# Kernel tuning notes

Measured on AMD Instinct MI355X. Metric: run time of the kernel, lower is better.

Reference implementation:

```python
import jax, jax.numpy as jnp
import numpy as np

N_P, E_P = 50000, 400000
N_L, E_L = 50000, 400000
B = 256  # number of graphs per side
NEG_GAT = 0.2   # GATv2 leaky-relu slope
NEG_FC = 0.01   # nn.LeakyReLU default slope


def _gatv2(x, ei, Wl, Wr, att, b, H, C):
    """GATv2Conv (concat heads, add_self_loops=True). Wl/Wr: [in, H*C], att: [H, C], b: [H*C]."""
    N = x.shape[0]
    sl = jnp.arange(N)
    src = jnp.concatenate([ei[0], sl])
    dst = jnp.concatenate([ei[1], sl])
    xl = (x @ Wl).reshape(N, H, C)   # source transform (messages)
    xr = (x @ Wr).reshape(N, H, C)   # target transform
    e = jax.nn.leaky_relu(xl[src] + xr[dst], NEG_GAT)          # [E+N, H, C]
    logits = jnp.einsum('ehc,hc->eh', e, att)                   # [E+N, H]
    m = jax.ops.segment_max(logits, dst, num_segments=N)        # segment softmax
    a = jnp.exp(logits - m[dst])
    alpha = a / jax.ops.segment_sum(a, dst, num_segments=N)[dst]
    out = jax.ops.segment_sum(xl[src] * alpha[..., None], dst, num_segments=N)
    return out.reshape(N, H * C) + b


def _mean_pool(x, batch, nb):
    s = jax.ops.segment_sum(x, batch, num_segments=nb)
    c = jax.ops.segment_sum(jnp.ones((x.shape[0],), x.dtype), batch, num_segments=nb)
    return s / jnp.maximum(c, 1.0)[:, None]


def setup_inputs() -> dict:
    key = jax.random.key(0)
    ks = jax.random.split(key, 48)
    i = [0]
    def nrm(shape, fan_in):
        k = ks[i[0]]; i[0] += 1
        return jax.random.normal(k, shape, jnp.float32) / np.sqrt(fan_in)
    inp = {}
    inp['protein_x'] = jax.random.normal(ks[40], (N_P, 10), jnp.float32)
    inp['ligand_x'] = jax.random.normal(ks[41], (N_L, 5), jnp.float32)
    inp['protein_edge_index'] = jax.random.randint(ks[42], (2, E_P), 0, N_P)
    inp['ligand_edge_index'] = jax.random.randint(ks[43], (2, E_L), 0, N_L)
    inp['protein_batch'] = (jnp.arange(N_P) * B) // N_P  # sorted graph ids, all segments nonempty
    inp['ligand_batch'] = (jnp.arange(N_L) * B) // N_L
    # GATv2 params: layer1 heads=2 out=128, layer2 heads=1 out=256
    inp['p1_Wl'] = nrm((10, 256), 10); inp['p1_Wr'] = nrm((10, 256), 10)
    inp['p1_att'] = nrm((2, 128), 128); inp['p1_b'] = jnp.zeros((256,), jnp.float32)
    inp['p2_Wl'] = nrm((256, 256), 256); inp['p2_Wr'] = nrm((256, 256), 256)
    inp['p2_att'] = nrm((1, 256), 256); inp['p2_b'] = jnp.zeros((256,), jnp.float32)
    inp['l1_Wl'] = nrm((5, 256), 5); inp['l1_Wr'] = nrm((5, 256), 5)
    inp['l1_att'] = nrm((2, 128), 128); inp['l1_b'] = jnp.zeros((256,), jnp.float32)
    inp['l2_Wl'] = nrm((256, 256), 256); inp['l2_Wr'] = nrm((256, 256), 256)
    inp['l2_att'] = nrm((1, 256), 256); inp['l2_b'] = jnp.zeros((256,), jnp.float32)
    # MultiheadAttention(256, 4) params ([in, out] convention)
    inp['Wq'] = nrm((256, 256), 256); inp['bq'] = jnp.zeros((256,), jnp.float32)
    inp['Wk'] = nrm((256, 256), 256); inp['bk'] = jnp.zeros((256,), jnp.float32)
    inp['Wv'] = nrm((256, 256), 256); inp['bv'] = jnp.zeros((256,), jnp.float32)
    inp['Wo'] = nrm((256, 256), 256); inp['bo'] = jnp.zeros((256,), jnp.float32)
    # fc head
    inp['fc1_w'] = nrm((512, 256), 512); inp['fc1_b'] = jnp.zeros((256,), jnp.float32)
    inp['ln_g'] = jnp.ones((256,), jnp.float32); inp['ln_b'] = jnp.zeros((256,), jnp.float32)
    inp['fc2_w'] = nrm((256, 1), 256); inp['fc2_b'] = jnp.zeros((1,), jnp.float32)
    return inp


def reference(protein_x, protein_edge_index, protein_batch,
              ligand_x, ligand_edge_index, ligand_batch,
              p1_Wl, p1_Wr, p1_att, p1_b, p2_Wl, p2_Wr, p2_att, p2_b,
              l1_Wl, l1_Wr, l1_att, l1_b, l2_Wl, l2_Wr, l2_att, l2_b,
              Wq, bq, Wk, bk, Wv, bv, Wo, bo,
              fc1_w, fc1_b, ln_g, ln_b, fc2_w, fc2_b):
    px = _gatv2(protein_x, protein_edge_index, p1_Wl, p1_Wr, p1_att, p1_b, 2, 128)
    px = _gatv2(px, protein_edge_index, p2_Wl, p2_Wr, p2_att, p2_b, 1, 256)
    px = _mean_pool(px, protein_batch, B)                        # [B, 256]
    lx = _gatv2(ligand_x, ligand_edge_index, l1_Wl, l1_Wr, l1_att, l1_b, 2, 128)
    lx = _gatv2(lx, ligand_edge_index, l2_Wl, l2_Wr, l2_att, l2_b, 1, 256)
    lx = _mean_pool(lx, ligand_batch, B)                         # [B, 256]
    # cross attention with q/k/v seq length 1
    D, H = 256, 4
    d = D // H
    qh = (px @ Wq + bq).reshape(B, H, d)
    kh = (lx @ Wk + bk).reshape(B, H, d)
    vh = (lx @ Wv + bv).reshape(B, H, d)
    scores = (qh * kh).sum(-1) / jnp.sqrt(jnp.float32(d))        # [B, H], 1 key
    w = jax.nn.softmax(scores[..., None], axis=-1)               # all ones (single key)
    attn = (w * vh).reshape(B, D) @ Wo + bo                      # [B, 256]
    comb = jnp.concatenate([px, attn], axis=1)                   # [B, 512]
    h = comb @ fc1_w + fc1_b
    mu = h.mean(-1, keepdims=True)
    var = h.var(-1, keepdims=True)
    h = (h - mu) / jnp.sqrt(var + 1e-5) * ln_g + ln_b
    h = jax.nn.leaky_relu(h, NEG_FC)
    return h @ fc2_w + fc2_b                                     # [B, 1]
```

## Files before the change

### kernel.cpp

```cpp
#include <hip/hip_runtime.h>
#include <math.h>

typedef unsigned short u16;
typedef __attribute__((ext_vector_type(8))) short bf16x8;
typedef __attribute__((ext_vector_type(4))) float f32x4;

__device__ inline u16 f2bf(float x) {
  unsigned int u = __float_as_uint(x);
  u += 0x7fffu + ((u >> 16) & 1u);
  return (u16)(u >> 16);
}
__device__ inline float bf2f(u16 h) {
  return __uint_as_float(((unsigned int)h) << 16);
}
__device__ inline float4 ld_bf4(const u16* p) {
  ushort4 v = *(const ushort4*)p;
  return make_float4(bf2f(v.x), bf2f(v.y), bf2f(v.z), bf2f(v.w));
}

__global__ void k_setup(int* __restrict__ cnt, int nz,
                        const float* __restrict__ Wpl, const float* __restrict__ Wpr,
                        const float* __restrict__ Wll, const float* __restrict__ Wlr,
                        u16* __restrict__ Whp, u16* __restrict__ Wlp,
                        u16* __restrict__ Whl, u16* __restrict__ Wll_o) {
  const int zb = (nz + 255) / 256;
  if ((int)blockIdx.x < zb) {
    int i = blockIdx.x * 256 + threadIdx.x;
    if (i < nz) cnt[i] = 0;
    return;
  }
  int wb = blockIdx.x - zb;
  int n = wb & 511;
  int side = wb >> 9;
  int col = n & 255;
  int k = threadIdx.x;
  const float* W = side == 0 ? (n < 256 ? Wpl : Wpr) : (n < 256 ? Wll : Wlr);
  float w = W[k * 256 + col];
  u16* Wh = side ? Whl : Whp;
  u16* Wlo = side ? Wll_o : Wlp;
  u16 hb = f2bf(w);
  Wh[n * 256 + k] = hb;
  Wlo[n * 256 + k] = f2bf(w - bf2f(hb));
}

__global__ void k_histb(const int* __restrict__ eip, int Ep, const int* __restrict__ eil,
                        int El, int* __restrict__ cntp, int* __restrict__ cntl) {
  int e = blockIdx.x * blockDim.x + threadIdx.x;
  if (e < Ep) atomicAdd(&cntp[eip[Ep + e]], 1);
  else if (e < Ep + El) { int e2 = e - Ep; atomicAdd(&cntl[eil[El + e2]], 1); }
}

__global__ void k_scan1b(const int* __restrict__ cntp, int Np, const int* __restrict__ cntl,
                         int Nl, int nbp, int* __restrict__ offsp, int* __restrict__ offsl,
                         int* __restrict__ curp, int* __restrict__ curl,
                         int* __restrict__ bsum) {
  __shared__ int s[256];
  int tid = threadIdx.x;
  int side = ((int)blockIdx.x >= nbp) ? 1 : 0;
  int blk = side ? (blockIdx.x - nbp) : blockIdx.x;
  const int* cnt = side ? cntl : cntp;
  int* offs = side ? offsl : offsp;
  int* cur = side ? curl : curp;
  int N = side ? Nl : Np;
  int i = blk * 256 + tid;
  int v = (i < N) ? cnt[i] : 0;
  if (i < N) cur[i] = 0;
  s[tid] = v;
  __syncthreads();
  for (int off = 1; off < 256; off <<= 1) {
    int t = 0;
    if (tid >= off) t = s[tid - off];
    __syncthreads();
    if (tid >= off) s[tid] += t;
    __syncthreads();
  }
  if (i < N) offs[i] = s[tid] - v;
  if (tid == 255) bsum[side * 256 + blk] = s[255];
}

__global__ void k_scan2b(int* __restrict__ bsum, int nbp, int nbl) {
  __shared__ int s[256];
  int side = blockIdx.x;
  int nb = side ? nbl : nbp;
  int* bs = bsum + side * 256;
  int tid = threadIdx.x;
  int v = (tid < nb) ? bs[tid] : 0;
  s[tid] = v;
  __syncthreads();
  for (int off = 1; off < 256; off <<= 1) {
    int t = 0;
    if (tid >= off) t = s[tid - off];
    __syncthreads();
    if (tid >= off) s[tid] += t;
    __syncthreads();
  }
  if (tid < nb) bs[tid] = s[tid] - v;
}

__global__ void k_fillb(const int* __restrict__ eip, int Ep, const int* __restrict__ eil,
                        int El, const int* __restrict__ offsp, const int* __restrict__ offsl,
                        const int* __restrict__ bsum,
                        int* __restrict__ curp, int* __restrict__ curl,
                        int* __restrict__ csrp, int* __restrict__ csrl) {
  int e = blockIdx.x * blockDim.x + threadIdx.x;
  if (e < Ep) {
    int d = eip[Ep + e];
    int pos = offsp[d] + bsum[d >> 8] + atomicAdd(&curp[d], 1);
    csrp[pos] = eip[e];
  } else if (e < Ep + El) {
    int e2 = e - Ep;
    int d = eil[El + e2];
    int pos = offsl[d] + bsum[256 + (d >> 8)] + atomicAdd(&curl[d], 1);
    csrl[pos] = eil[e2];
  }
}

__global__ void k_lin_small_b(const float* __restrict__ xp, int Kp, int Np,
                              const float* __restrict__ xl_, int Kl, int Nl,
                              const float* __restrict__ Wpl, const float* __restrict__ Wpr,
                              const float* __restrict__ Wll, const float* __restrict__ Wlr,
                              u16* __restrict__ xlh_p, u16* __restrict__ xrh_p,
                              u16* __restrict__ xlh_l, u16* __restrict__ xrh_l) {
  const int side = blockIdx.y;
  const float* x = side ? xl_ : xp;
  const int K = side ? Kl : Kp;
  const int N = side ? Nl : Np;
  const float* Wl = side ? Wll : Wpl;
  const float* Wr = side ? Wlr : Wpr;
  u16* xlh = side ? xlh_l : xlh_p;
  u16* xrh = side ? xrh_l : xrh_p;
  int base = blockIdx.x * 8;
  if (base >= N) return;
  int j = threadIdx.x;
  __shared__ float xs[8][16];
  int tot = 8 * K;
  for (int i = j; i < tot; i += 256) {
    int r = i / K, k = i - r * K;
    if (base + r < N) xs[r][k] = x[(size_t)(base + r) * K + k];
  }
  __syncthreads();
#pragma unroll
  for (int r = 0; r < 8; ++r) {
    int n = base + r;
    if (n >= N) break;
    float al = 0.f, ar = 0.f;
    for (int k = 0; k < K; ++k) {
      float xv = xs[r][k];
      al = fmaf(xv, Wl[k * 256 + j], al);
      ar = fmaf(xv, Wr[k * 256 + j], ar);
    }
    xlh[(size_t)n * 256 + j] = f2bf(al);
    xrh[(size_t)n * 256 + j] = f2bf(ar);
  }
}

__global__ void __launch_bounds__(256, 2) k_mm_dual_b(
    const u16* __restrict__ A_p, const u16* __restrict__ A_l,
    const u16* __restrict__ Bh_p, const u16* __restrict__ Bl_p,
    const u16* __restrict__ Bh_l, const u16* __restrict__ Bl_l,
    u16* __restrict__ XLh_p, u16* __restrict__ XRh_p,
    u16* __restrict__ XLh_l, u16* __restrict__ XRh_l, int Np, int Nl) {
  __shared__ __align__(16) char smem[32768];
  char* sA = smem;
  char* sBh = smem + 8192;
  char* sBl = smem + 16384;
  const int side = blockIdx.z;
  const u16* A = side ? A_l : A_p;
  const u16* Bhi = side ? Bh_l : Bh_p;
  const u16* Blo = side ? Bl_l : Bl_p;
  u16* XLh = side ? XLh_l : XLh_p;
  u16* XRh = side ? XRh_l : XRh_p;
  const int M = side ? Nl : Np;
  const int t = threadIdx.x;
  const int rowBase = blockIdx.x * 128;
  if (rowBase >= M) return;
  const int j0 = blockIdx.y * 128;
  const int srow = t >> 1;
  const int h = t & 1;
  int gr = rowBase + srow;
  if (gr >= M) gr = M - 1;
  const size_t gaBase = (size_t)gr * 256 + h * 16;
  const size_t gbBase = (size_t)(j0 + srow) * 256 + h * 16;
  const int rb = srow * 64;
  const int sw0 = (((h * 2) + (srow >> 1)) & 3) * 16;
  const int sw1 = (((h * 2 + 1) + (srow >> 1)) & 3) * 16;
  const int lane = t & 63;
  const int wid = t >> 6;
  const int wm = (wid & 1) * 64;
  const int wn = (wid >> 1) * 64;
  const int kq = lane >> 4;
  const int mr = lane & 15;
  int offA[4], offB[4];
#pragma unroll
  for (int i = 0; i < 4; ++i) {
    int m = wm + i * 16 + mr;
    offA[i] = m * 64 + ((kq + (m >> 1)) & 3) * 16;
    int n = wn + i * 16 + mr;
    offB[i] = n * 64 + ((kq + (n >> 1)) & 3) * 16;
  }
  f32x4 acc[4][4] = {};
  for (int kt = 0; kt < 8; ++kt) {
    const int k0 = kt * 32;
    uint4 va0 = *(const uint4*)(A + gaBase + k0);
    uint4 va1 = *(const uint4*)(A + gaBase + k0 + 8);
    uint4 vbh0 = *(const uint4*)(Bhi + gbBase + k0);
    uint4 vbh1 = *(const uint4*)(Bhi + gbBase + k0 + 8);
    uint4 vbl0 = *(const uint4*)(Blo + gbBase + k0);
    uint4 vbl1 = *(const uint4*)(Blo + gbBase + k0 + 8);
    __syncthreads();
    *(uint4*)(sA + rb + sw0) = va0;
    *(uint4*)(sA + rb + sw1) = va1;
    *(uint4*)(sBh + rb + sw0) = vbh0;
    *(uint4*)(sBh + rb + sw1) = vbh1;
    *(uint4*)(sBl + rb + sw0) = vbl0;
    *(uint4*)(sBl + rb + sw1) = vbl1;
    __syncthreads();
    bf16x8 a[4], bh[4], bl[4];
#pragma unroll
    for (int i = 0; i < 4; ++i) {
      a[i] = *(const bf16x8*)(sA + offA[i]);
      bh[i] = *(const bf16x8*)(sBh + offB[i]);
      bl[i] = *(const bf16x8*)(sBl + offB[i]);
    }
#pragma unroll
    for (int i = 0; i < 4; ++i)
#pragma unroll
      for (int j = 0; j < 4; ++j) {
        acc[i][j] = __builtin_amdgcn_mfma_f32_16x16x32_bf16(a[i], bh[j], acc[i][j], 0, 0, 0);
        acc[i][j] = __builtin_amdgcn_mfma_f32_16x16x32_bf16(a[i], bl[j], acc[i][j], 0, 0, 0);
      }
  }
  __syncthreads();
  u16* wtile = (u16*)(smem + wid * 8192);
#pragma unroll
  for (int i = 0; i < 4; ++i)
#pragma unroll
    for (int j = 0; j < 4; ++j)
#pragma unroll
      for (int r = 0; r < 4; ++r)
        wtile[(i * 16 + kq * 4 + r) * 64 + j * 16 + mr] = f2bf(acc[i][j][r]);
  u16* cbase = (blockIdx.y < 2) ? XLh : XRh;
  const int cb = (blockIdx.y < 2) ? j0 : j0 - 256;
  const int r8 = lane >> 3;
  const int c8 = lane & 7;
#pragma unroll
  for (int rr = 0; rr < 8; ++rr) {
    int lr = rr * 8 + r8;
    uint4 v = *(const uint4*)&wtile[lr * 64 + c8 * 8];
    int row = rowBase + wm + lr;
    if (row < M) *(uint4*)&cbase[(size_t)row * 256 + cb + wn + c8 * 8] = v;
  }
}

#define GAT_DOT(a, q)                                                        \
  {                                                                          \
    float t0 = a.x + rd.x, t1 = a.y + rd.y, t2 = a.z + rd.z, t3 = a.w + rd.w; \
    q = fmaf(fmaxf(t0, 0.2f * t0), wa.x,                                     \
        fmaf(fmaxf(t1, 0.2f * t1), wa.y,                                     \
        fmaf(fmaxf(t2, 0.2f * t2), wa.z, fmaxf(t3, 0.2f * t3) * wa.w)));     \
  }

template <int H>
__global__ void k_gat_gather_b(
    const u16* __restrict__ xlh_p, const u16* __restrict__ xrh_p, u16* __restrict__ out_p,
    const u16* __restrict__ xlh_l, const u16* __restrict__ xrh_l, u16* __restrict__ out_l,
    const int* __restrict__ csr_p, const int* __restrict__ offs_p,
    const int* __restrict__ cnt_p,
    const int* __restrict__ csr_l, const int* __restrict__ offs_l,
    const int* __restrict__ cnt_l, const int* __restrict__ bsum,
    const float* __restrict__ att_p, const float* __restrict__ bias_p,
    const float* __restrict__ att_l, const float* __restrict__ bias_l,
    int Np, int Nl) {
  const int side = blockIdx.y;
  const u16* xlh = side ? xlh_l : xlh_p;
  const u16* xrh = side ? xrh_l : xrh_p;
  u16* out = side ? out_l : out_p;
  const int* csr = side ? csr_l : csr_p;
  const int* offs = side ? offs_l : offs_p;
  const int* cnt = side ? cnt_l : cnt_p;
  const float* att = side ? att_l : att_p;
  const float* bias = side ? bias_l : bias_p;
  const int N = side ? Nl : Np;
  int d = blockIdx.x * 4 + (threadIdx.x >> 6);
  if (d >= N) return;
  const int lo4 = (threadIdx.x & 63) * 4;
  const float4 rd = ld_bf4(&xrh[(size_t)d * 256 + lo4]);
  const float4 wa = *(const float4*)&att[lo4];
  const float4 xd = ld_bf4(&xlh[(size_t)d * 256 + lo4]);
  float base;
  GAT_DOT(xd, base)
#pragma unroll
  for (int off = 1; off <= (H == 2 ? 16 : 32); off <<= 1) base += __shfl_xor(base, off, 64);
  float l0 = 1.f, l1 = 0.f, l2 = 0.f, l3 = 0.f;
  float4 acc0 = xd;
  float4 acc1 = make_float4(0.f, 0.f, 0.f, 0.f);
  float4 acc2 = make_float4(0.f, 0.f, 0.f, 0.f);
  float4 acc3 = make_float4(0.f, 0.f, 0.f, 0.f);
  const int o0 = offs[d] + bsum[side * 256 + (d >> 8)];
  const int c = cnt[d];
  int j = 0;
  for (; j + 3 < c; j += 4) {
    int s0 = csr[o0 + j], s1 = csr[o0 + j + 1], s2 = csr[o0 + j + 2], s3 = csr[o0 + j + 3];
    float4 a0 = ld_bf4(&xlh[(size_t)s0 * 256 + lo4]);
    float4 a1 = ld_bf4(&xlh[(size_t)s1 * 256 + lo4]);
    float4 a2 = ld_bf4(&xlh[(size_t)s2 * 256 + lo4]);
    float4 a3 = ld_bf4(&xlh[(size_t)s3 * 256 + lo4]);
    float q0, q1, q2, q3;
    GAT_DOT(a0, q0)
    GAT_DOT(a1, q1)
    GAT_DOT(a2, q2)
    GAT_DOT(a3, q3)
#pragma unroll
    for (int off = 1; off <= (H == 2 ? 16 : 32); off <<= 1) {
      q0 += __shfl_xor(q0, off, 64);
      q1 += __shfl_xor(q1, off, 64);
      q2 += __shfl_xor(q2, off, 64);
      q3 += __shfl_xor(q3, off, 64);
    }
    float w0 = __expf(q0 - base), w1 = __expf(q1 - base);
    float w2 = __expf(q2 - base), w3 = __expf(q3 - base);
    l0 += w0; l1 += w1; l2 += w2; l3 += w3;
    acc0.x = fmaf(w0, a0.x, acc0.x); acc0.y = fmaf(w0, a0.y, acc0.y);
    acc0.z = fmaf(w0, a0.z, acc0.z); acc0.w = fmaf(w0, a0.w, acc0.w);
    acc1.x = fmaf(w1, a1.x, acc1.x); acc1.y = fmaf(w1, a1.y, acc1.y);
    acc1.z = fmaf(w1, a1.z, acc1.z); acc1.w = fmaf(w1, a1.w, acc1.w);
    acc2.x = fmaf(w2, a2.x, acc2.x); acc2.y = fmaf(w2, a2.y, acc2.y);
    acc2.z = fmaf(w2, a2.z, acc2.z); acc2.w = fmaf(w2, a2.w, acc2.w);
    acc3.x = fmaf(w3, a3.x, acc3.x); acc3.y = fmaf(w3, a3.y, acc3.y);
    acc3.z = fmaf(w3, a3.z, acc3.z); acc3.w = fmaf(w3, a3.w, acc3.w);
  }
  for (; j < c; ++j) {
    int s0 = csr[o0 + j];
    float4 a0 = ld_bf4(&xlh[(size_t)s0 * 256 + lo4]);
    float q0;
    GAT_DOT(a0, q0)
#pragma unroll
    for (int off = 1; off <= (H == 2 ? 16 : 32); off <<= 1) q0 += __shfl_xor(q0, off, 64);
    float w0 = __expf(q0 - base);
    l0 += w0;
    acc0.x = fmaf(w0, a0.x, acc0.x); acc0.y = fmaf(w0, a0.y, acc0.y);
    acc0.z = fmaf(w0, a0.z, acc0.z); acc0.w = fmaf(w0, a0.w, acc0.w);
  }
  float inv = 1.f / (l0 + l1 + l2 + l3);
  float ax = acc0.x + acc1.x + acc2.x + acc3.x;
  float ay = acc0.y + acc1.y + acc2.y + acc3.y;
  float az = acc0.z + acc1.z + acc2.z + acc3.z;
  float aw = acc0.w + acc1.w + acc2.w + acc3.w;
  const float4 b4 = *(const float4*)&bias[lo4];
  ushort4 hv;
  hv.x = f2bf(ax * inv + b4.x);
  hv.y = f2bf(ay * inv + b4.y);
  hv.z = f2bf(az * inv + b4.z);
  hv.w = f2bf(aw * inv + b4.w);
  *(ushort4*)&out[(size_t)d * 256 + lo4] = hv;
}

#define POOL_C 8
__global__ void k_pool_part(const u16* __restrict__ xp, const int* __restrict__ bp, int Np,
                            const u16* __restrict__ xl_, const int* __restrict__ bl_, int Nl,
                            float* __restrict__ PPpart, float* __restrict__ LPpart) {
  const int b = blockIdx.x;
  const int side = blockIdx.y;
  const int chunk = blockIdx.z;
  const u16* x = side ? xl_ : xp;
  const int* batch = side ? bl_ : bp;
  const int N = side ? Nl : Np;
  float* part = side ? LPpart : PPpart;
  int j = threadIdx.x;
  __shared__ int sss, sse;
  if (j == 0) {
    int lo = 0, hi = N;
    while (lo < hi) { int mid = (lo + hi) >> 1; if (batch[mid] < b) lo = mid + 1; else hi = mid; }
    sss = lo;
    lo = 0; hi = N;
    while (lo < hi) { int mid = (lo + hi) >> 1; if (batch[mid] < b + 1) lo = mid + 1; else hi = mid; }
    sse = lo;
  }
  __syncthreads();
  int len = sse - sss;
  int per = (len + POOL_C - 1) / POOL_C;
  int st = sss + chunk * per;
  int en = st + per;
  if (en > sse) en = sse;
  float acc = 0.f;
  for (int n = st; n < en; ++n) acc += bf2f(x[(size_t)n * 256 + j]);
  part[((size_t)chunk * 256 + b) * 256 + j] = acc;
}

__global__ void k_head(const float* __restrict__ PPpart, const float* __restrict__ LPpart,
                       const int* __restrict__ bp, int Np,
                       const int* __restrict__ bl_, int Nl,
                       const float* __restrict__ Wv, const float* __restrict__ bv,
                       const float* __restrict__ Wo, const float* __restrict__ bo,
                       const float* __restrict__ fc1w, const float* __restrict__ fc1b,
                       const float* __restrict__ lng, const float* __restrict__ lnb,
                       const float* __restrict__ fc2w, const float* __restrict__ fc2b,
                       float* __restrict__ out) {
  int b = blockIdx.x;
  int j = threadIdx.x;
  __shared__ float lxs[256];
  __shared__ float vbuf[256];
  __shared__ float comb[512];
  __shared__ float r1[256], r2[256];
  __shared__ float smu, srs;
  __shared__ int seg[4];
  if (j < 2) {
    const int* batch = j ? bl_ : bp;
    int N = j ? Nl : Np;
    int lo = 0, hi = N;
    while (lo < hi) { int mid = (lo + hi) >> 1; if (batch[mid] < b) lo = mid + 1; else hi = mid; }
    seg[j * 2] = lo;
    lo = 0; hi = N;
    while (lo < hi) { int mid = (lo + hi) >> 1; if (batch[mid] < b + 1) lo = mid + 1; else hi = mid; }
    seg[j * 2 + 1] = lo;
  }
  __syncthreads();
  {
    float accp = 0.f, accl = 0.f;
#pragma unroll
    for (int c = 0; c < POOL_C; ++c) {
      accp += PPpart[((size_t)c * 256 + b) * 256 + j];
      accl += LPpart[((size_t)c * 256 + b) * 256 + j];
    }
    comb[j] = accp / fmaxf((float)(seg[1] - seg[0]), 1.f);
    lxs[j] = accl / fmaxf((float)(seg[3] - seg[2]), 1.f);
  }
  __syncthreads();
  float v = bv[j];
  for (int k = 0; k < 256; ++k) v = fmaf(lxs[k], Wv[k * 256 + j], v);
  vbuf[j] = v;
  __syncthreads();
  float at = bo[j];
  for (int k = 0; k < 256; ++k) at = fmaf(vbuf[k], Wo[k * 256 + j], at);
  comb[256 + j] = at;
  __syncthreads();
  float h = fc1b[j];
  for (int k = 0; k < 512; ++k) h = fmaf(comb[k], fc1w[k * 256 + j], h);
  r1[j] = h;
  r2[j] = h * h;
  __syncthreads();
  for (int off = 128; off > 0; off >>= 1) {
    if (j < off) { r1[j] += r1[j + off]; r2[j] += r2[j + off]; }
    __syncthreads();
  }
  if (j == 0) {
    float mu = r1[0] / 256.f;
    float var = r2[0] / 256.f - mu * mu;
    smu = mu;
    srs = 1.f / sqrtf(var + 1e-5f);
  }
  __syncthreads();
  float hn = (h - smu) * srs * lng[j] + lnb[j];
  hn = hn > 0.f ? hn : 0.01f * hn;
  r1[j] = hn * fc2w[j];
  __syncthreads();
  for (int off = 128; off > 0; off >>= 1) {
    if (j < off) r1[j] += r1[j + off];
    __syncthreads();
  }
  if (j == 0) out[b] = r1[0] + fc2b[0];
}

extern "C" void kernel_launch(void* const* d_in, const int* in_sizes, int n_in,
                              void* d_out, int out_size, void* d_ws, size_t ws_size,
                              hipStream_t stream) {
  const float* px = (const float*)d_in[0];
  const float* lx = (const float*)d_in[1];
  const int* pei = (const int*)d_in[2];
  const int* lei = (const int*)d_in[3];
  const int* pb = (const int*)d_in[4];
  const int* lb = (const int*)d_in[5];
  const float* p1_Wl = (const float*)d_in[6];
  const float* p1_Wr = (const float*)d_in[7];
  const float* p1_att = (const float*)d_in[8];
  const float* p1_b = (const float*)d_in[9];
  const float* p2_Wl = (const float*)d_in[10];
  const float* p2_Wr = (const float*)d_in[11];
  const float* p2_att = (const float*)d_in[12];
  const float* p2_b = (const float*)d_in[13];
  const float* l1_Wl = (const float*)d_in[14];
  const float* l1_Wr = (const float*)d_in[15];
  const float* l1_att = (const float*)d_in[16];
  const float* l1_b = (const float*)d_in[17];
  const float* l2_Wl = (const float*)d_in[18];
  const float* l2_Wr = (const float*)d_in[19];
  const float* l2_att = (const float*)d_in[20];
  const float* l2_b = (const float*)d_in[21];
  const float* Wv = (const float*)d_in[26];
  const float* bv = (const float*)d_in[27];
  const float* Wo = (const float*)d_in[28];
  const float* bo = (const float*)d_in[29];
  const float* fc1w = (const float*)d_in[30];
  const float* fc1b = (const float*)d_in[31];
  const float* lng = (const float*)d_in[32];
  const float* lnb = (const float*)d_in[33];
  const float* fc2w = (const float*)d_in[34];
  const float* fc2b = (const float*)d_in[35];

  const int NPn = in_sizes[4];
  const int NLn = in_sizes[5];
  const int EPe = in_sizes[2] / 2;
  const int ELe = in_sizes[3] / 2;
  const int KP = in_sizes[0] / NPn;
  const int KL = in_sizes[1] / NLn;

  const int Nmax = NPn > NLn ? NPn : NLn;
  const int Emax = EPe > ELe ? EPe : ELe;
  size_t NF = (size_t)Nmax * 256;

  u16* XLh_p = (u16*)d_ws;
  u16* XRh_p = XLh_p + NF;
  u16* Ah_p = XRh_p + NF;
  u16* XLh_l = Ah_p + NF;
  u16* XRh_l = XLh_l + NF;
  u16* Ah_l = XRh_l + NF;
  u16* Wth = Ah_l + NF;
  u16* Wtl = Wth + 2 * 512 * 256;
  float* PPpart = (float*)(Wtl + 2 * 512 * 256);
  float* LPpart = PPpart + (size_t)POOL_C * 256 * 256;
  int* cnt = (int*)(LPpart + (size_t)POOL_C * 256 * 256);
  int* cur = cnt + 2 * (size_t)Nmax;
  int* offs = cur + 2 * (size_t)Nmax;
  int* bsum = offs + 2 * (size_t)Nmax;
  int* csr = bsum + 512;
  int* cnt_l = cnt + Nmax;
  int* cur_l = cur + Nmax;
  int* offs_l = offs + Nmax;
  int* csr_l = csr + Emax;

  const int nbp = (NPn + 255) / 256;
  const int nbl = (NLn + 255) / 256;
  const int nz = 2 * Nmax;
  const int zb = (nz + 255) / 256;

  k_setup<<<zb + 1024, 256, 0, stream>>>(cnt, nz, p2_Wl, p2_Wr, l2_Wl, l2_Wr,
                                         Wth, Wtl, Wth + 512 * 256, Wtl + 512 * 256);
  k_histb<<<(EPe + ELe + 255) / 256, 256, 0, stream>>>(pei, EPe, lei, ELe, cnt, cnt_l);
  k_scan1b<<<nbp + nbl, 256, 0, stream>>>(cnt, NPn, cnt_l, NLn, nbp, offs, offs_l,
                                          cur, cur_l, bsum);
  k_scan2b<<<2, 256, 0, stream>>>(bsum, nbp, nbl);
  k_fillb<<<(EPe + ELe + 255) / 256, 256, 0, stream>>>(pei, EPe, lei, ELe, offs, offs_l,
                                                       bsum, cur, cur_l, csr, csr_l);
  k_lin_small_b<<<dim3((Nmax + 7) / 8, 2), 256, 0, stream>>>(
      px, KP, NPn, lx, KL, NLn, p1_Wl, p1_Wr, l1_Wl, l1_Wr,
      XLh_p, XRh_p, XLh_l, XRh_l);
  k_gat_gather_b<2><<<dim3((Nmax + 3) / 4, 2), 256, 0, stream>>>(
      XLh_p, XRh_p, Ah_p, XLh_l, XRh_l, Ah_l,
      csr, offs, cnt, csr_l, offs_l, cnt_l, bsum,
      p1_att, p1_b, l1_att, l1_b, NPn, NLn);
  k_mm_dual_b<<<dim3((Nmax + 127) / 128, 4, 2), 256, 0, stream>>>(
      Ah_p, Ah_l, Wth, Wtl, Wth + 512 * 256, Wtl + 512 * 256,
      XLh_p, XRh_p, XLh_l, XRh_l, NPn, NLn);
  k_gat_gather_b<1><<<dim3((Nmax + 3) / 4, 2), 256, 0, stream>>>(
      XLh_p, XRh_p, Ah_p, XLh_l, XRh_l, Ah_l,
      csr, offs, cnt, csr_l, offs_l, cnt_l, bsum,
      p2_att, p2_b, l2_att, l2_b, NPn, NLn);
  k_pool_part<<<dim3(256, 2, POOL_C), 256, 0, stream>>>(Ah_p, pb, NPn, Ah_l, lb, NLn,
                                                        PPpart, LPpart);
  k_head<<<256, 256, 0, stream>>>(PPpart, LPpart, pb, NPn, lb, NLn,
                                  Wv, bv, Wo, bo, fc1w, fc1b, lng, lnb, fc2w, fc2b,
                                  (float*)d_out);
  (void)n_in; (void)out_size; (void)ws_size;
}
```

Before: 596.8 us.

## Vectorize GAT gather to 8-wide loads, fuse small linear into setup, swizzle GEMM grid

```diff
diff --git a/kernel.cpp b/kernel.cpp
--- a/kernel.cpp
+++ b/kernel.cpp
@@ -13,16 +13,32 @@
 __device__ inline float bf2f(u16 h) {
   return __uint_as_float(((unsigned int)h) << 16);
 }
-__device__ inline float4 ld_bf4(const u16* p) {
-  ushort4 v = *(const ushort4*)p;
-  return make_float4(bf2f(v.x), bf2f(v.y), bf2f(v.z), bf2f(v.w));
+__device__ inline void cvt8(uint4 v, float4& A, float4& B) {
+  A.x = __uint_as_float(v.x << 16);
+  A.y = __uint_as_float(v.x & 0xffff0000u);
+  A.z = __uint_as_float(v.y << 16);
+  A.w = __uint_as_float(v.y & 0xffff0000u);
+  B.x = __uint_as_float(v.z << 16);
+  B.y = __uint_as_float(v.z & 0xffff0000u);
+  B.z = __uint_as_float(v.w << 16);
+  B.w = __uint_as_float(v.w & 0xffff0000u);
+}
+__device__ inline unsigned int pk2bf(float lo, float hi) {
+  return (unsigned int)f2bf(lo) | ((unsigned int)f2bf(hi) << 16);
 }
 
 __global__ void k_setup(int* __restrict__ cnt, int nz,
-                        const float* __restrict__ Wpl, const float* __restrict__ Wpr,
-                        const float* __restrict__ Wll, const float* __restrict__ Wlr,
+                        const float* __restrict__ W2pl, const float* __restrict__ W2pr,
+                        const float* __restrict__ W2ll, const float* __restrict__ W2lr,
                         u16* __restrict__ Whp, u16* __restrict__ Wlp,
-                        u16* __restrict__ Whl, u16* __restrict__ Wll_o) {
+                        u16* __restrict__ Whl, u16* __restrict__ Wll_o,
+                        const float* __restrict__ xp, int Kp, int Np,
+                        const float* __restrict__ xl_, int Kl, int Nl,
+                        const float* __restrict__ W1pl, const float* __restrict__ W1pr,
+                        const float* __restrict__ W1ll, const float* __restrict__ W1lr,
+                        u16* __restrict__ xlh_p, u16* __restrict__ xrh_p,
+                        u16* __restrict__ xlh_l, u16* __restrict__ xrh_l,
+                        int linPer) {
   const int zb = (nz + 255) / 256;
   if ((int)blockIdx.x < zb) {
     int i = blockIdx.x * 256 + threadIdx.x;
@@ -30,17 +46,52 @@
     return;
   }
   int wb = blockIdx.x - zb;
-  int n = wb & 511;
-  int side = wb >> 9;
-  int col = n & 255;
-  int k = threadIdx.x;
-  const float* W = side == 0 ? (n < 256 ? Wpl : Wpr) : (n < 256 ? Wll : Wlr);
-  float w = W[k * 256 + col];
-  u16* Wh = side ? Whl : Whp;
-  u16* Wlo = side ? Wll_o : Wlp;
-  u16 hb = f2bf(w);
-  Wh[n * 256 + k] = hb;
-  Wlo[n * 256 + k] = f2bf(w - bf2f(hb));
+  if (wb < 1024) {
+    int n = wb & 511;
+    int side = wb >> 9;
+    int col = n & 255;
+    int k = threadIdx.x;
+    const float* W = side == 0 ? (n < 256 ? W2pl : W2pr) : (n < 256 ? W2ll : W2lr);
+    float w = W[k * 256 + col];
+    u16* Wh = side ? Whl : Whp;
+    u16* Wlo = side ? Wll_o : Wlp;
+    u16 hb = f2bf(w);
+    Wh[n * 256 + k] = hb;
+    Wlo[n * 256 + k] = f2bf(w - bf2f(hb));
+    return;
+  }
+  int wb2 = wb - 1024;
+  const int side = wb2 / linPer;
+  const float* x = side ? xl_ : xp;
+  const int K = side ? Kl : Kp;
+  const int N = side ? Nl : Np;
+  const float* Wl = side ? W1ll : W1pl;
+  const float* Wr = side ? W1lr : W1pr;
+  u16* xlh = side ? xlh_l : xlh_p;
+  u16* xrh = side ? xrh_l : xrh_p;
+  int base = (wb2 - side * linPer) * 8;
+  if (base >= N) return;
+  int j = threadIdx.x;
+  __shared__ float xs[8][16];
+  int tot = 8 * K;
+  for (int i = j; i < tot; i += 256) {
+    int r = i / K, k = i - r * K;
+    if (base + r < N) xs[r][k] = x[(size_t)(base + r) * K + k];
+  }
+  __syncthreads();
+#pragma unroll
+  for (int r = 0; r < 8; ++r) {
+    int n = base + r;
+    if (n >= N) break;
+    float al = 0.f, ar = 0.f;
+    for (int k = 0; k < K; ++k) {
+      float xv = xs[r][k];
+      al = fmaf(xv, Wl[k * 256 + j], al);
+      ar = fmaf(xv, Wr[k * 256 + j], ar);
+    }
+    xlh[(size_t)n * 256 + j] = f2bf(al);
+    xrh[(size_t)n * 256 + j] = f2bf(ar);
+  }
 }
 
 __global__ void k_histb(const int* __restrict__ eip, int Ep, const int* __restrict__ eil,
@@ -115,56 +166,22 @@
   }
 }
 
-__global__ void k_lin_small_b(const float* __restrict__ xp, int Kp, int Np,
-                              const float* __restrict__ xl_, int Kl, int Nl,
-                              const float* __restrict__ Wpl, const float* __restrict__ Wpr,
-                              const float* __restrict__ Wll, const float* __restrict__ Wlr,
-                              u16* __restrict__ xlh_p, u16* __restrict__ xrh_p,
-                              u16* __restrict__ xlh_l, u16* __restrict__ xrh_l) {
-  const int side = blockIdx.y;
-  const float* x = side ? xl_ : xp;
-  const int K = side ? Kl : Kp;
-  const int N = side ? Nl : Np;
-  const float* Wl = side ? Wll : Wpl;
-  const float* Wr = side ? Wlr : Wpr;
-  u16* xlh = side ? xlh_l : xlh_p;
-  u16* xrh = side ? xrh_l : xrh_p;
-  int base = blockIdx.x * 8;
-  if (base >= N) return;
-  int j = threadIdx.x;
-  __shared__ float xs[8][16];
-  int tot = 8 * K;
-  for (int i = j; i < tot; i += 256) {
-    int r = i / K, k = i - r * K;
-    if (base + r < N) xs[r][k] = x[(size_t)(base + r) * K + k];
-  }
-  __syncthreads();
-#pragma unroll
-  for (int r = 0; r < 8; ++r) {
-    int n = base + r;
-    if (n >= N) break;
-    float al = 0.f, ar = 0.f;
-    for (int k = 0; k < K; ++k) {
-      float xv = xs[r][k];
-      al = fmaf(xv, Wl[k * 256 + j], al);
-      ar = fmaf(xv, Wr[k * 256 + j], ar);
-    }
-    xlh[(size_t)n * 256 + j] = f2bf(al);
-    xrh[(size_t)n * 256 + j] = f2bf(ar);
-  }
-}
-
 __global__ void __launch_bounds__(256, 2) k_mm_dual_b(
     const u16* __restrict__ A_p, const u16* __restrict__ A_l,
     const u16* __restrict__ Bh_p, const u16* __restrict__ Bl_p,
     const u16* __restrict__ Bh_l, const u16* __restrict__ Bl_l,
     u16* __restrict__ XLh_p, u16* __restrict__ XRh_p,
-    u16* __restrict__ XLh_l, u16* __restrict__ XRh_l, int Np, int Nl) {
+    u16* __restrict__ XLh_l, u16* __restrict__ XRh_l, int Np, int Nl, int Rp, int Rtot) {
   __shared__ __align__(16) char smem[32768];
   char* sA = smem;
   char* sBh = smem + 8192;
   char* sBl = smem + 16384;
-  const int side = blockIdx.z;
+  const int gid = blockIdx.x;
+  const int rblk = (gid >> 5) * 8 + (gid & 7);
+  const int col = (gid >> 3) & 3;
+  if (rblk >= Rtot) return;
+  const int side = (rblk >= Rp) ? 1 : 0;
+  const int rloc = side ? rblk - Rp : rblk;
   const u16* A = side ? A_l : A_p;
   const u16* Bhi = side ? Bh_l : Bh_p;
   const u16* Blo = side ? Bl_l : Bl_p;
@@ -172,9 +189,8 @@
   u16* XRh = side ? XRh_l : XRh_p;
   const int M = side ? Nl : Np;
   const int t = threadIdx.x;
-  const int rowBase = blockIdx.x * 128;
-  if (rowBase >= M) return;
-  const int j0 = blockIdx.y * 128;
+  const int rowBase = rloc * 128;
+  const int j0 = col * 128;
   const int srow = t >> 1;
   const int h = t & 1;
   int gr = rowBase + srow;
@@ -239,8 +255,8 @@
 #pragma unroll
       for (int r = 0; r < 4; ++r)
         wtile[(i * 16 + kq * 4 + r) * 64 + j * 16 + mr] = f2bf(acc[i][j][r]);
-  u16* cbase = (blockIdx.y < 2) ? XLh : XRh;
-  const int cb = (blockIdx.y < 2) ? j0 : j0 - 256;
+  u16* cbase = (col < 2) ? XLh : XRh;
+  const int cb = (col < 2) ? j0 : j0 - 256;
   const int r8 = lane >> 3;
   const int c8 = lane & 7;
 #pragma unroll
@@ -252,12 +268,24 @@
   }
 }
 
-#define GAT_DOT(a, q)                                                        \
-  {                                                                          \
-    float t0 = a.x + rd.x, t1 = a.y + rd.y, t2 = a.z + rd.z, t3 = a.w + rd.w; \
-    q = fmaf(fmaxf(t0, 0.2f * t0), wa.x,                                     \
-        fmaf(fmaxf(t1, 0.2f * t1), wa.y,                                     \
-        fmaf(fmaxf(t2, 0.2f * t2), wa.z, fmaxf(t3, 0.2f * t3) * wa.w)));     \
+#define DOT8(A0, A1, q)                                                       \
+  {                                                                           \
+    float t;                                                                  \
+    t = A0.x + rd0.x; q = fmaf(t, s60.x, fabsf(t) * s40.x);                   \
+    t = A0.y + rd0.y; q = fmaf(fabsf(t), s40.y, fmaf(t, s60.y, q));           \
+    t = A0.z + rd0.z; q = fmaf(fabsf(t), s40.z, fmaf(t, s60.z, q));           \
+    t = A0.w + rd0.w; q = fmaf(fabsf(t), s40.w, fmaf(t, s60.w, q));           \
+    t = A1.x + rd1.x; q = fmaf(fabsf(t), s41.x, fmaf(t, s61.x, q));           \
+    t = A1.y + rd1.y; q = fmaf(fabsf(t), s41.y, fmaf(t, s61.y, q));           \
+    t = A1.z + rd1.z; q = fmaf(fabsf(t), s41.z, fmaf(t, s61.z, q));           \
+    t = A1.w + rd1.w; q = fmaf(fabsf(t), s41.w, fmaf(t, s61.w, q));           \
+  }
+
+#define RED(q)                                                                \
+  {                                                                           \
+    _Pragma("unroll")                                                         \
+    for (int off = 1; off <= (H == 2 ? 8 : 16); off <<= 1)                    \
+      q += __shfl_xor(q, off, 64);                                            \
   }
 
 template <int H>
@@ -283,76 +311,98 @@
   const int N = side ? Nl : Np;
   int d = blockIdx.x * 4 + (threadIdx.x >> 6);
   if (d >= N) return;
-  const int lo4 = (threadIdx.x & 63) * 4;
-  const float4 rd = ld_bf4(&xrh[(size_t)d * 256 + lo4]);
-  const float4 wa = *(const float4*)&att[lo4];
-  const float4 xd = ld_bf4(&xlh[(size_t)d * 256 + lo4]);
+  const int lane = threadIdx.x & 63;
+  const int half = lane >> 5;
+  const int cb = (lane & 31) * 8;
+  float4 rd0, rd1, xd0, xd1;
+  {
+    uint4 rv = *(const uint4*)&xrh[(size_t)d * 256 + cb];
+    cvt8(rv, rd0, rd1);
+    uint4 xv = *(const uint4*)&xlh[(size_t)d * 256 + cb];
+    cvt8(xv, xd0, xd1);
+  }
+  const float4 wa0 = *(const float4*)&att[cb];
+  const float4 wa1 = *(const float4*)&att[cb + 4];
+  const float4 s60 = make_float4(0.6f * wa0.x, 0.6f * wa0.y, 0.6f * wa0.z, 0.6f * wa0.w);
+  const float4 s61 = make_float4(0.6f * wa1.x, 0.6f * wa1.y, 0.6f * wa1.z, 0.6f * wa1.w);
+  const float4 s40 = make_float4(0.4f * wa0.x, 0.4f * wa0.y, 0.4f * wa0.z, 0.4f * wa0.w);
+  const float4 s41 = make_float4(0.4f * wa1.x, 0.4f * wa1.y, 0.4f * wa1.z, 0.4f * wa1.w);
   float base;
-  GAT_DOT(xd, base)
-#pragma unroll
-  for (int off = 1; off <= (H == 2 ? 16 : 32); off <<= 1) base += __shfl_xor(base, off, 64);
-  float l0 = 1.f, l1 = 0.f, l2 = 0.f, l3 = 0.f;
-  float4 acc0 = xd;
-  float4 acc1 = make_float4(0.f, 0.f, 0.f, 0.f);
-  float4 acc2 = make_float4(0.f, 0.f, 0.f, 0.f);
-  float4 acc3 = make_float4(0.f, 0.f, 0.f, 0.f);
+  DOT8(xd0, xd1, base)
+  RED(base)
+  float lA = half ? 0.f : 1.f, lB = 0.f;
+  float4 aA0 = half ? make_float4(0.f, 0.f, 0.f, 0.f) : xd0;
+  float4 aA1 = half ? make_float4(0.f, 0.f, 0.f, 0.f) : xd1;
+  float4 aB0 = make_float4(0.f, 0.f, 0.f, 0.f);
+  float4 aB1 = make_float4(0.f, 0.f, 0.f, 0.f);
   const int o0 = offs[d] + bsum[side * 256 + (d >> 8)];
   const int c = cnt[d];
   int j = 0;
   for (; j + 3 < c; j += 4) {
-    int s0 = csr[o0 + j], s1 = csr[o0 + j + 1], s2 = csr[o0 + j + 2], s3 = csr[o0 + j + 3];
-    float4 a0 = ld_bf4(&xlh[(size_t)s0 * 256 + lo4]);
-    float4 a1 = ld_bf4(&xlh[(size_t)s1 * 256 + lo4]);
-    float4 a2 = ld_bf4(&xlh[(size_t)s2 * 256 + lo4]);
-    float4 a3 = ld_bf4(&xlh[(size_t)s3 * 256 + lo4]);
-    float q0, q1, q2, q3;
-    GAT_DOT(a0, q0)
-    GAT_DOT(a1, q1)
-    GAT_DOT(a2, q2)
-    GAT_DOT(a3, q3)
-#pragma unroll
-    for (int off = 1; off <= (H == 2 ? 16 : 32); off <<= 1) {
-      q0 += __shfl_xor(q0, off, 64);
-      q1 += __shfl_xor(q1, off, 64);
-      q2 += __shfl_xor(q2, off, 64);
-      q3 += __shfl_xor(q3, off, 64);
-    }
-    float w0 = __expf(q0 - base), w1 = __expf(q1 - base);
-    float w2 = __expf(q2 - base), w3 = __expf(q3 - base);
-    l0 += w0; l1 += w1; l2 += w2; l3 += w3;
-    acc0.x = fmaf(w0, a0.x, acc0.x); acc0.y = fmaf(w0, a0.y, acc0.y);
-    acc0.z = fmaf(w0, a0.z, acc0.z); acc0.w = fmaf(w0, a0.w, acc0.w);
-    acc1.x = fmaf(w1, a1.x, acc1.x); acc1.y = fmaf(w1, a1.y, acc1.y);
-    acc1.z = fmaf(w1, a1.z, acc1.z); acc1.w = fmaf(w1, a1.w, acc1.w);
-    acc2.x = fmaf(w2, a2.x, acc2.x); acc2.y = fmaf(w2, a2.y, acc2.y);
-    acc2.z = fmaf(w2, a2.z, acc2.z); acc2.w = fmaf(w2, a2.w, acc2.w);
-    acc3.x = fmaf(w3, a3.x, acc3.x); acc3.y = fmaf(w3, a3.y, acc3.y);
-    acc3.z = fmaf(w3, a3.z, acc3.z); acc3.w = fmaf(w3, a3.w, acc3.w);
-  }
-  for (; j < c; ++j) {
-    int s0 = csr[o0 + j];
-    float4 a0 = ld_bf4(&xlh[(size_t)s0 * 256 + lo4]);
-    float q0;
-    GAT_DOT(a0, q0)
-#pragma unroll
-    for (int off = 1; off <= (H == 2 ? 16 : 32); off <<= 1) q0 += __shfl_xor(q0, off, 64);
-    float w0 = __expf(q0 - base);
-    l0 += w0;
-    acc0.x = fmaf(w0, a0.x, acc0.x); acc0.y = fmaf(w0, a0.y, acc0.y);
-    acc0.z = fmaf(w0, a0.z, acc0.z); acc0.w = fmaf(w0, a0.w, acc0.w);
-  }
-  float inv = 1.f / (l0 + l1 + l2 + l3);
-  float ax = acc0.x + acc1.x + acc2.x + acc3.x;
-  float ay = acc0.y + acc1.y + acc2.y + acc3.y;
-  float az = acc0.z + acc1.z + acc2.z + acc3.z;
-  float aw = acc0.w + acc1.w + acc2.w + acc3.w;
-  const float4 b4 = *(const float4*)&bias[lo4];
-  ushort4 hv;
-  hv.x = f2bf(ax * inv + b4.x);
-  hv.y = f2bf(ay * inv + b4.y);
-  hv.z = f2bf(az * inv + b4.z);
-  hv.w = f2bf(aw * inv + b4.w);
-  *(ushort4*)&out[(size_t)d * 256 + lo4] = hv;
+    int sA = csr[o0 + j + half];
+    int sB = csr[o0 + j + 2 + half];
+    uint4 vA = *(const uint4*)&xlh[(size_t)sA * 256 + cb];
+    uint4 vB = *(const uint4*)&xlh[(size_t)sB * 256 + cb];
+    float4 a0, a1, b0, b1;
+    cvt8(vA, a0, a1);
+    cvt8(vB, b0, b1);
+    float qA, qB;
+    DOT8(a0, a1, qA)
+    DOT8(b0, b1, qB)
+    RED(qA)
+    RED(qB)
+    float wA = __expf(qA - base), wB = __expf(qB - base);
+    lA += wA; lB += wB;
+    aA0.x = fmaf(wA, a0.x, aA0.x); aA0.y = fmaf(wA, a0.y, aA0.y);
+    aA0.z = fmaf(wA, a0.z, aA0.z); aA0.w = fmaf(wA, a0.w, aA0.w);
+    aA1.x = fmaf(wA, a1.x, aA1.x); aA1.y = fmaf(wA, a1.y, aA1.y);
+    aA1.z = fmaf(wA, a1.z, aA1.z); aA1.w = fmaf(wA, a1.w, aA1.w);
+    aB0.x = fmaf(wB, b0.x, aB0.x); aB0.y = fmaf(wB, b0.y, aB0.y);
+    aB0.z = fmaf(wB, b0.z, aB0.z); aB0.w = fmaf(wB, b0.w, aB0.w);
+    aB1.x = fmaf(wB, b1.x, aB1.x); aB1.y = fmaf(wB, b1.y, aB1.y);
+    aB1.z = fmaf(wB, b1.z, aB1.z); aB1.w = fmaf(wB, b1.w, aB1.w);
+  }
+  for (; j < c; j += 2) {
+    int e = j + half;
+    bool valid = e < c;
+    int sA = valid ? csr[o0 + e] : 0;
+    uint4 vA = *(const uint4*)&xlh[(size_t)sA * 256 + cb];
+    float4 a0, a1;
+    cvt8(vA, a0, a1);
+    float qA;
+    DOT8(a0, a1, qA)
+    RED(qA)
+    float wA = valid ? __expf(qA - base) : 0.f;
+    lA += wA;
+    aA0.x = fmaf(wA, a0.x, aA0.x); aA0.y = fmaf(wA, a0.y, aA0.y);
+    aA0.z = fmaf(wA, a0.z, aA0.z); aA0.w = fmaf(wA, a0.w, aA0.w);
+    aA1.x = fmaf(wA, a1.x, aA1.x); aA1.y = fmaf(wA, a1.y, aA1.y);
+    aA1.z = fmaf(wA, a1.z, aA1.z); aA1.w = fmaf(wA, a1.w, aA1.w);
+  }
+  float l = lA + lB;
+  float4 a0, a1;
+  a0.x = aA0.x + aB0.x; a0.y = aA0.y + aB0.y; a0.z = aA0.z + aB0.z; a0.w = aA0.w + aB0.w;
+  a1.x = aA1.x + aB1.x; a1.y = aA1.y + aB1.y; a1.z = aA1.z + aB1.z; a1.w = aA1.w + aB1.w;
+  l += __shfl_xor(l, 32, 64);
+  a0.x += __shfl_xor(a0.x, 32, 64);
+  a0.y += __shfl_xor(a0.y, 32, 64);
+  a0.z += __shfl_xor(a0.z, 32, 64);
+  a0.w += __shfl_xor(a0.w, 32, 64);
+  a1.x += __shfl_xor(a1.x, 32, 64);
+  a1.y += __shfl_xor(a1.y, 32, 64);
+  a1.z += __shfl_xor(a1.z, 32, 64);
+  a1.w += __shfl_xor(a1.w, 32, 64);
+  if (half == 0) {
+    float inv = 1.f / l;
+    const float4 b0 = *(const float4*)&bias[cb];
+    const float4 b1 = *(const float4*)&bias[cb + 4];
+    uint4 ov;
+    ov.x = pk2bf(a0.x * inv + b0.x, a0.y * inv + b0.y);
+    ov.y = pk2bf(a0.z * inv + b0.z, a0.w * inv + b0.w);
+    ov.z = pk2bf(a1.x * inv + b1.x, a1.y * inv + b1.y);
+    ov.w = pk2bf(a1.z * inv + b1.z, a1.w * inv + b1.w);
+    *(uint4*)&out[(size_t)d * 256 + cb] = ov;
+  }
 }
 
 #define POOL_C 8
@@ -532,25 +582,31 @@
   const int nbl = (NLn + 255) / 256;
   const int nz = 2 * Nmax;
   const int zb = (nz + 255) / 256;
-
-  k_setup<<<zb + 1024, 256, 0, stream>>>(cnt, nz, p2_Wl, p2_Wr, l2_Wl, l2_Wr,
-                                         Wth, Wtl, Wth + 512 * 256, Wtl + 512 * 256);
+  const int linPer = (Nmax + 7) / 8;
+
+  k_setup<<<zb + 1024 + 2 * linPer, 256, 0, stream>>>(
+      cnt, nz, p2_Wl, p2_Wr, l2_Wl, l2_Wr,
+      Wth, Wtl, Wth + 512 * 256, Wtl + 512 * 256,
+      px, KP, NPn, lx, KL, NLn, p1_Wl, p1_Wr, l1_Wl, l1_Wr,
+      XLh_p, XRh_p, XLh_l, XRh_l, linPer);
   k_histb<<<(EPe + ELe + 255) / 256, 256, 0, stream>>>(pei, EPe, lei, ELe, cnt, cnt_l);
   k_scan1b<<<nbp + nbl, 256, 0, stream>>>(cnt, NPn, cnt_l, NLn, nbp, offs, offs_l,
                                           cur, cur_l, bsum);
   k_scan2b<<<2, 256, 0, stream>>>(bsum, nbp, nbl);
   k_fillb<<<(EPe + ELe + 255) / 256, 256, 0, stream>>>(pei, EPe, lei, ELe, offs, offs_l,
                                                        bsum, cur, cur_l, csr, csr_l);
-  k_lin_small_b<<<dim3((Nmax + 7) / 8, 2), 256, 0, stream>>>(
-      px, KP, NPn, lx, KL, NLn, p1_Wl, p1_Wr, l1_Wl, l1_Wr,
-      XLh_p, XRh_p, XLh_l, XRh_l);
   k_gat_gather_b<2><<<dim3((Nmax + 3) / 4, 2), 256, 0, stream>>>(
       XLh_p, XRh_p, Ah_p, XLh_l, XRh_l, Ah_l,
       csr, offs, cnt, csr_l, offs_l, cnt_l, bsum,
       p1_att, p1_b, l1_att, l1_b, NPn, NLn);
-  k_mm_dual_b<<<dim3((Nmax + 127) / 128, 4, 2), 256, 0, stream>>>(
-      Ah_p, Ah_l, Wth, Wtl, Wth + 512 * 256, Wtl + 512 * 256,
-      XLh_p, XRh_p, XLh_l, XRh_l, NPn, NLn);
+  {
+    const int Rp = (NPn + 127) / 128;
+    const int Rl = (NLn + 127) / 128;
+    const int Rtot = Rp + Rl;
+    k_mm_dual_b<<<32 * ((Rtot + 7) / 8), 256, 0, stream>>>(
+        Ah_p, Ah_l, Wth, Wtl, Wth + 512 * 256, Wtl + 512 * 256,
+        XLh_p, XRh_p, XLh_l, XRh_l, NPn, NLn, Rp, Rtot);
+  }
   k_gat_gather_b<1><<<dim3((Nmax + 3) / 4, 2), 256, 0, stream>>>(
       XLh_p, XRh_p, Ah_p, XLh_l, XRh_l, Ah_l,
       csr, offs, cnt, csr_l, offs_l, cnt_l, bsum,
```

After: 587.6 us. No clear change (-1.6%).
